# Optimization experiments

Measured on AMD Instinct MI355X. Metric: run time of the kernel, lower is better.

The kernel has to match this reference:

```python
import jax, jax.numpy as jnp
import numpy as np

B, T = 32, 48
INPUT_DIM = 40000
TRAJ = 10
H = 256
OUT = 40000
TD = 48
L = 2
E = 128
DIN = E + TD  # 176


def setup_inputs() -> dict:
    key = jax.random.key(0)
    ks = jax.random.split(key, 16)
    s = 0.05
    inp = {
        "locations": jax.random.randint(ks[0], (B, T), 0, INPUT_DIM),
        "times": jax.random.randint(ks[1], (B, T), 0, TD),
        "labels": jax.random.randint(ks[2], (B,), 0, TRAJ),
        "embed_table": jax.random.normal(ks[3], (INPUT_DIM, E), dtype=jnp.float32) * s,
        "traj_table": jax.random.normal(ks[4], (TRAJ, H * L), dtype=jnp.float32) * s,
        "fc_w": jax.random.normal(ks[5], (OUT + TD, H), dtype=jnp.float32) * s,
        "fc_b": jnp.zeros((OUT + TD,), dtype=jnp.float32),
        "w_ih0": jax.random.normal(ks[6], (3 * H, DIN), dtype=jnp.float32) * s,
        "w_hh0": jax.random.normal(ks[7], (3 * H, H), dtype=jnp.float32) * s,
        "b_ih0": jnp.zeros((3 * H,), dtype=jnp.float32),
        "b_hh0": jnp.zeros((3 * H,), dtype=jnp.float32),
        "w_ih1": jax.random.normal(ks[8], (3 * H, H), dtype=jnp.float32) * s,
        "w_hh1": jax.random.normal(ks[9], (3 * H, H), dtype=jnp.float32) * s,
        "b_ih1": jnp.zeros((3 * H,), dtype=jnp.float32),
        "b_hh1": jnp.zeros((3 * H,), dtype=jnp.float32),
    }
    return inp


def gru_layer(x, h0, w_ih, w_hh, b_ih, b_hh):
    """PyTorch-semantics GRU layer. x: [T,B,din], h0: [B,H] -> [T,B,H]."""
    # precompute input projections for all timesteps (gates ordered r,z,n)
    xp = jnp.einsum('tbd,gd->tbg', x, w_ih) + b_ih  # [T,B,3H]

    def step(h, xp_t):
        hp = h @ w_hh.T + b_hh                      # [B,3H]
        xr, xz, xn = jnp.split(xp_t, 3, axis=-1)
        hr, hz, hn = jnp.split(hp, 3, axis=-1)
        r = jax.nn.sigmoid(xr + hr)
        z = jax.nn.sigmoid(xz + hz)
        n = jnp.tanh(xn + r * hn)
        h_new = (1.0 - z) * n + z * h
        return h_new, h_new

    _, ys = jax.lax.scan(step, h0, xp)
    return ys


def reference(locations, times, labels, embed_table, traj_table, fc_w, fc_b,
              w_ih0, w_hh0, b_ih0, b_hh0, w_ih1, w_hh1, b_ih1, b_hh1):
    x = embed_table[locations]                                  # [B,T,E]
    th = jax.nn.one_hot(times, TD, dtype=x.dtype)               # [B,T,TD]
    x = jnp.concatenate([x, th], axis=-1).transpose(1, 0, 2)    # [T,B,E+TD]
    # init_hidden: view (B, L*H) -> (L, -1, H), a raw reshape as in torch
    h0 = traj_table[labels].reshape(L, -1, H)                   # [L,B,H]
    y = gru_layer(x, h0[0], w_ih0, w_hh0, b_ih0, b_hh0)
    y = gru_layer(y, h0[1], w_ih1, w_hh1, b_ih1, b_hh1)         # [T,B,H]
    out = jax.nn.relu(y).transpose(1, 0, 2) @ fc_w.T + fc_b     # [B,T,OUT+TD]
    loc = jax.nn.log_softmax(out[..., :OUT], axis=-1)
    tm = jax.nn.log_softmax(out[..., OUT:], axis=-1)
    return loc, tm
```

## Files before the change

### kernel.cpp

```cpp
#include <hip/hip_runtime.h>
#include <math.h>

typedef __attribute__((ext_vector_type(4))) float f32x4;
typedef __attribute__((ext_vector_type(8))) short s16x8;

constexpr int B = 32, T = 48, H = 256, E = 128, TD = 48;
constexpr int OUT = 40000, NOUTC = 40048, NPADC = 40064;
constexpr int G3 = 768, DIN = 176;

__device__ __forceinline__ float sigmoidf_(float x){ return 1.f/(1.f+__expf(-x)); }
__device__ __forceinline__ float tanhf_(float x){
  float e = __expf(2.f*x);
  return 1.f - 2.f/(e + 1.f);
}
__device__ __forceinline__ unsigned short f2bf(float f){
  unsigned int u = __float_as_uint(f);
  u += 0x7fffu + ((u>>16)&1u);
  return (unsigned short)(u>>16);
}
__device__ __forceinline__ s16x8 pack8(float4 u, float4 v){
  s16x8 r;
  r[0]=(short)f2bf(u.x); r[1]=(short)f2bf(u.y); r[2]=(short)f2bf(u.z); r[3]=(short)f2bf(u.w);
  r[4]=(short)f2bf(v.x); r[5]=(short)f2bf(v.y); r[6]=(short)f2bf(v.z); r[7]=(short)f2bf(v.w);
  return r;
}
__device__ __forceinline__ void gl_lds16(const unsigned short* g, unsigned short* l){
  __builtin_amdgcn_global_load_lds((const __attribute__((address_space(1))) void*)g,
                                   (__attribute__((address_space(3))) void*)l, 16, 0, 0);
}
__device__ __forceinline__ void st_sc(unsigned* p, unsigned v){
  __hip_atomic_store(p, v, __ATOMIC_RELAXED, __HIP_MEMORY_SCOPE_SYSTEM);
}
__device__ __forceinline__ unsigned long long ld_sc64(const unsigned long long* p){
  return __hip_atomic_load(p, __ATOMIC_RELAXED, __HIP_MEMORY_SCOPE_SYSTEM);
}

__global__ void wt_kernel(const float* __restrict__ w_ih0, float* __restrict__ wT,
                          unsigned* __restrict__ bar){
  int i = blockIdx.x*256 + threadIdx.x;
  if (blockIdx.x == 0 && threadIdx.x == 0)
    __hip_atomic_store(bar, 0u, __ATOMIC_RELAXED, __HIP_MEMORY_SCOPE_SYSTEM);
  if (i >= E*G3) return;
  int e = i / G3, g = i % G3;
  wT[i] = w_ih0[g*DIN + e];
}

__global__ void xp0_kernel(const int* __restrict__ locations, const int* __restrict__ times,
                           const float* __restrict__ embed, const float* __restrict__ wT,
                           const float* __restrict__ w_ih0, const float* __restrict__ b_ih0,
                           float* __restrict__ xp0)
{
  __shared__ float emb_s[16][E];
  __shared__ int tm_s[16];
  const int r0 = blockIdx.x * 16;
  const int tid = threadIdx.x;
  for (int i = tid; i < 16*E; i += 256) {
    int p = i >> 7, e = i & 127;
    int r = r0 + p; int t = r >> 5, b = r & 31;
    emb_s[p][e] = embed[(size_t)locations[b*T + t]*E + e];
  }
  if (tid < 16) {
    int r = r0 + tid; int t = r >> 5, b = r & 31;
    tm_s[tid] = times[b*T + t];
  }
  __syncthreads();
  const int g = tid;
  float acc[16][3];
  #pragma unroll
  for (int p=0;p<16;p++){acc[p][0]=0.f;acc[p][1]=0.f;acc[p][2]=0.f;}
  for (int e = 0; e < E; e += 4) {
    float w0_[4], w1_[4], w2_[4];
    #pragma unroll
    for (int i=0;i<4;i++){
      w0_[i]=wT[(e+i)*G3 + g];
      w1_[i]=wT[(e+i)*G3 + 256 + g];
      w2_[i]=wT[(e+i)*G3 + 512 + g];
    }
    #pragma unroll
    for (int p=0;p<16;p++){
      float4 ev = *(const float4*)&emb_s[p][e];
      acc[p][0] += ev.x*w0_[0]+ev.y*w0_[1]+ev.z*w0_[2]+ev.w*w0_[3];
      acc[p][1] += ev.x*w1_[0]+ev.y*w1_[1]+ev.z*w1_[2]+ev.w*w1_[3];
      acc[p][2] += ev.x*w2_[0]+ev.y*w2_[1]+ev.z*w2_[2]+ev.w*w2_[3];
    }
  }
  #pragma unroll
  for (int p=0;p<16;p++){
    int r = r0+p; int tt = tm_s[p];
    xp0[(size_t)r*G3 + g]       = acc[p][0] + b_ih0[g]     + w_ih0[g*DIN       + E + tt];
    xp0[(size_t)r*G3 + 256 + g] = acc[p][1] + b_ih0[g+256] + w_ih0[(g+256)*DIN + E + tt];
    xp0[(size_t)r*G3 + 512 + g] = acc[p][2] + b_ih0[g+512] + w_ih0[(g+512)*DIN + E + tt];
  }
}

struct GruArgs {
  const float* xp0; const float* traj; const int* labels;
  const float* w_hh0; const float* b_hh0;
  const float* w_ih1; const float* w_hh1; const float* b_ih1; const float* b_hh1;
  unsigned short* exch;
  unsigned* bar;
  unsigned short* abf;
};

__global__ void __launch_bounds__(384, 2) gru_kernel(GruArgs a)
{
  __shared__ unsigned short Ash[2][32*264];
  __shared__ float gl0[3*32*17];
  __shared__ float gl1[4*32*17];
  __shared__ float hF0[512];
  __shared__ float hF1[512];
  const int tid  = threadIdx.x;
  const int jt   = blockIdx.x;
  const int wv   = tid >> 6;
  const int lane = tid & 63;
  const int g    = wv % 3, mt = wv / 3;
  const int fn   = lane & 15;
  const int fq   = lane >> 4;
  unsigned* exch32 = (unsigned*)a.exch;

  const int row = g*256 + jt*16 + fn;
  s16x8 b0[8], b1[16];
  #pragma unroll
  for (int kk = 0; kk < 8; ++kk) {
    const float* p0 = a.w_hh0 + (size_t)row*H + kk*32 + fq*8;
    const float* p1 = a.w_ih1 + (size_t)row*H + kk*32 + fq*8;
    const float* p2 = a.w_hh1 + (size_t)row*H + kk*32 + fq*8;
    b0[kk]    = pack8(*(const float4*)p0, *(const float4*)(p0+4));
    b1[kk]    = pack8(*(const float4*)p1, *(const float4*)(p1+4));
    b1[kk+8]  = pack8(*(const float4*)p2, *(const float4*)(p2+4));
  }

  for (int i = tid; i < 2*B*H; i += 384) {
    int l = i >> 13, bb = (i >> 8) & 31, h = i & 255;
    float v = a.traj[(size_t)a.labels[l*16 + (bb>>1)]*512 + (bb&1)*256 + h];
    Ash[l][bb*264 + h] = f2bf(v);
  }
  if (tid < 256) {
    int b = tid >> 3, jp = tid & 7, j0 = jp*2, gj = jt*16 + j0;
    float v00 = a.traj[(size_t)a.labels[(b>>1)]*512      + (b&1)*256 + gj];
    float v01 = a.traj[(size_t)a.labels[(b>>1)]*512      + (b&1)*256 + gj+1];
    float v10 = a.traj[(size_t)a.labels[16 + (b>>1)]*512 + (b&1)*256 + gj];
    float v11 = a.traj[(size_t)a.labels[16 + (b>>1)]*512 + (b&1)*256 + gj+1];
    hF0[b*16+j0] = v00; hF0[b*16+j0+1] = v01;
    hF1[b*16+j0] = v10; hF1[b*16+j0+1] = v11;
    st_sc(&exch32[(1*2+1)*4096 + b*128 + jt*8 + jp],
          (unsigned)f2bf(v10) | ((unsigned)f2bf(v11) << 16));
  }

  for (int p = 0; p <= T; ++p) {
    const int cur = p & 1, nxt = cur ^ 1;
    if (p) {
      const unsigned long long* src = (const unsigned long long*)a.exch + (size_t)cur*4096;
      unsigned long long v[11];
      #pragma unroll
      for (int k = 0; k < 11; ++k) {
        int i = tid + k*384;
        if (i < 4096) v[k] = ld_sc64(&src[i]);
      }
      #pragma unroll
      for (int k = 0; k < 11; ++k) {
        int i = tid + k*384;
        if (i < 4096) {
          int st = i >> 11, bb = (i >> 6) & 31, k4 = (i & 63) << 2;
          *(unsigned long long*)&Ash[st][bb*264 + k4] = v[k];
        }
      }
    }
    __syncthreads();

    if (p < T) {
      f32x4 acc = (f32x4){0.f,0.f,0.f,0.f};
      #pragma unroll
      for (int kk = 0; kk < 8; ++kk) {
        s16x8 af = *(const s16x8*)&Ash[0][(mt*16 + fn)*264 + kk*32 + fq*8];
        acc = __builtin_amdgcn_mfma_f32_16x16x32_bf16(af, b0[kk], acc, 0, 0, 0);
      }
      #pragma unroll
      for (int i = 0; i < 4; ++i)
        gl0[(g*32 + mt*16 + fq*4 + i)*17 + fn] = acc[i];
    }
    if (p >= 1) {
      if (g < 2) {
        f32x4 acc = (f32x4){0.f,0.f,0.f,0.f};
        #pragma unroll
        for (int kk = 0; kk < 8; ++kk) {
          s16x8 af = *(const s16x8*)&Ash[0][(mt*16 + fn)*264 + kk*32 + fq*8];
          acc = __builtin_amdgcn_mfma_f32_16x16x32_bf16(af, b1[kk], acc, 0, 0, 0);
        }
        #pragma unroll
        for (int kk = 0; kk < 8; ++kk) {
          s16x8 af = *(const s16x8*)&Ash[1][(mt*16 + fn)*264 + kk*32 + fq*8];
          acc = __builtin_amdgcn_mfma_f32_16x16x32_bf16(af, b1[8+kk], acc, 0, 0, 0);
        }
        #pragma unroll
        for (int i = 0; i < 4; ++i)
          gl1[(g*32 + mt*16 + fq*4 + i)*17 + fn] = acc[i];
      } else {
        f32x4 ax = (f32x4){0.f,0.f,0.f,0.f}, ah = (f32x4){0.f,0.f,0.f,0.f};
        #pragma unroll
        for (int kk = 0; kk < 8; ++kk) {
          s16x8 afx = *(const s16x8*)&Ash[0][(mt*16 + fn)*264 + kk*32 + fq*8];
          s16x8 afh = *(const s16x8*)&Ash[1][(mt*16 + fn)*264 + kk*32 + fq*8];
          ax = __builtin_amdgcn_mfma_f32_16x16x32_bf16(afx, b1[kk],   ax, 0, 0, 0);
          ah = __builtin_amdgcn_mfma_f32_16x16x32_bf16(afh, b1[8+kk], ah, 0, 0, 0);
        }
        #pragma unroll
        for (int i = 0; i < 4; ++i) {
          gl1[(2*32 + mt*16 + fq*4 + i)*17 + fn] = ax[i];
          gl1[(3*32 + mt*16 + fq*4 + i)*17 + fn] = ah[i];
        }
      }
    }
    __syncthreads();

    if (tid < 256) {
      const int b = tid >> 3, jp = tid & 7, j0 = jp*2, gj = jt*16 + j0;
      if (p < T) {
        const float* xp = a.xp0 + (size_t)(p*B + b)*G3 + gj;
        float r0 = sigmoidf_(xp[0]   + gl0[(b)*17+j0]      + a.b_hh0[gj]);
        float r1 = sigmoidf_(xp[1]   + gl0[(b)*17+j0+1]    + a.b_hh0[gj+1]);
        float z0 = sigmoidf_(xp[256] + gl0[(32+b)*17+j0]   + a.b_hh0[256+gj]);
        float z1 = sigmoidf_(xp[257] + gl0[(32+b)*17+j0+1] + a.b_hh0[256+gj+1]);
        float n0 = tanhf_(xp[512] + r0*(gl0[(64+b)*17+j0]   + a.b_hh0[512+gj]));
        float n1 = tanhf_(xp[513] + r1*(gl0[(64+b)*17+j0+1] + a.b_hh0[512+gj+1]));
        float h0n = (1.f - z0)*n0 + z0*hF0[b*16+j0];
        float h1n = (1.f - z1)*n1 + z1*hF0[b*16+j0+1];
        hF0[b*16+j0] = h0n; hF0[b*16+j0+1] = h1n;
        st_sc(&exch32[(nxt*2 + 0)*4096 + b*128 + jt*8 + jp],
              (unsigned)f2bf(h0n) | ((unsigned)f2bf(h1n) << 16));
      }
      if (p >= 1) {
        const int t1 = p - 1;
        float r0 = sigmoidf_(gl1[(b)*17+j0]      + a.b_ih1[gj]     + a.b_hh1[gj]);
        float r1 = sigmoidf_(gl1[(b)*17+j0+1]    + a.b_ih1[gj+1]   + a.b_hh1[gj+1]);
        float z0 = sigmoidf_(gl1[(32+b)*17+j0]   + a.b_ih1[256+gj]   + a.b_hh1[256+gj]);
        float z1 = sigmoidf_(gl1[(32+b)*17+j0+1] + a.b_ih1[256+gj+1] + a.b_hh1[256+gj+1]);
        float n0 = tanhf_(gl1[(64+b)*17+j0]   + a.b_ih1[512+gj]
                          + r0*(gl1[(96+b)*17+j0]   + a.b_hh1[512+gj]));
        float n1 = tanhf_(gl1[(64+b)*17+j0+1] + a.b_ih1[512+gj+1]
                          + r1*(gl1[(96+b)*17+j0+1] + a.b_hh1[512+gj+1]));
        float h0n = (1.f - z0)*n0 + z0*hF1[b*16+j0];
        float h1n = (1.f - z1)*n1 + z1*hF1[b*16+j0+1];
        hF1[b*16+j0] = h0n; hF1[b*16+j0+1] = h1n;
        st_sc(&exch32[(nxt*2 + 1)*4096 + b*128 + jt*8 + jp],
              (unsigned)f2bf(h0n) | ((unsigned)f2bf(h1n) << 16));
        ((unsigned*)a.abf)[((size_t)(b*T + t1)*H + gj) >> 1] =
              (unsigned)f2bf(fmaxf(h0n,0.f)) | ((unsigned)f2bf(fmaxf(h1n,0.f)) << 16);
      }
    }
    if (p == T) break;

    asm volatile("s_waitcnt vmcnt(0)" ::: "memory");
    __syncthreads();
    if (tid == 0) {
      __hip_atomic_fetch_add(a.bar, 1u, __ATOMIC_RELAXED, __HIP_MEMORY_SCOPE_SYSTEM);
      const unsigned tgt = 16u*(unsigned)(p + 1);
      unsigned it = 0;
      while (__hip_atomic_load(a.bar, __ATOMIC_RELAXED, __HIP_MEMORY_SCOPE_SYSTEM) < tgt) {
        if (++it > (1u<<21)) break;
      }
    }
    __syncthreads();
  }
}

__global__ void castw_kernel(const float* __restrict__ fcw, unsigned short* __restrict__ wbf){
  int g = blockIdx.x*256 + threadIdx.x;
  if (g >= NPADC*64) return;
  int row = g >> 6;
  ushort4 o;
  if (row < NOUTC) {
    float4 v = ((const float4*)fcw)[g];
    o.x=f2bf(v.x); o.y=f2bf(v.y); o.z=f2bf(v.z); o.w=f2bf(v.w);
  } else { o.x=0; o.y=0; o.z=0; o.w=0; }
  ((ushort4*)wbf)[g] = o;
}

__global__ void __launch_bounds__(256) gemm_kernel(const unsigned short* __restrict__ Abf,
                                                   const unsigned short* __restrict__ Wbf,
                                                   const float* __restrict__ fc_b,
                                                   float* __restrict__ dout)
{
  __shared__ unsigned short As[128*32];
  __shared__ unsigned short Ws[128*32];
  const int m0 = blockIdx.x * 128;
  const int n0 = blockIdx.y * 128;
  const int tid = threadIdx.x;
  const int lane = tid & 63;
  const int wv = tid >> 6;
  f32x4 acc[2][8];
  #pragma unroll
  for (int i=0;i<2;i++)
    #pragma unroll
    for(int jx=0;jx<8;jx++) acc[i][jx] = (f32x4){0.f,0.f,0.f,0.f};

  const int srow = tid >> 2;
  const int skoff = (tid & 3) * 8;
  const unsigned short* aptr = Abf + (size_t)(m0 + srow)*256 + skoff;
  const unsigned short* wptr = Wbf + (size_t)(n0 + srow)*256 + skoff;
  unsigned short* asd = &As[tid*8];
  unsigned short* wsd = &Ws[tid*8];

  const int fr = lane & 15;
  const int fk = (lane >> 4) * 8;

  for (int kk = 0; kk < 256; kk += 32) {
    gl_lds16(aptr + kk,            asd);
    gl_lds16(aptr + 64*256 + kk,   asd + 64*32);
    gl_lds16(wptr + kk,            wsd);
    gl_lds16(wptr + 64*256 + kk,   wsd + 64*32);
    __syncthreads();
    s16x8 a0 = *(const s16x8*)&As[(wv*32 + fr)*32 + fk];
    s16x8 a1 = *(const s16x8*)&As[(wv*32 + 16 + fr)*32 + fk];
    #pragma unroll
    for (int ct = 0; ct < 8; ++ct) {
      s16x8 bfr = *(const s16x8*)&Ws[(ct*16 + fr)*32 + fk];
      acc[0][ct] = __builtin_amdgcn_mfma_f32_16x16x32_bf16(a0, bfr, acc[0][ct], 0, 0, 0);
      acc[1][ct] = __builtin_amdgcn_mfma_f32_16x16x32_bf16(a1, bfr, acc[1][ct], 0, 0, 0);
    }
    __syncthreads();
  }

  const int quad = lane >> 4;
  #pragma unroll
  for (int rt = 0; rt < 2; ++rt) {
    #pragma unroll
    for (int ct = 0; ct < 8; ++ct) {
      int col = n0 + ct*16 + fr;
      if (col < NOUTC) {
        float bias = fc_b[col];
        #pragma unroll
        for (int i = 0; i < 4; ++i) {
          int row = m0 + wv*32 + rt*16 + quad*4 + i;
          float v = acc[rt][ct][i] + bias;
          if (col < OUT) dout[(size_t)row*OUT + col] = v;
          else dout[(size_t)OUT*B*T + (size_t)row*TD + (col - OUT)] = v;
        }
      }
    }
  }
}

__global__ void stats_kernel(const float* __restrict__ dout, float* __restrict__ logz){
  const int r = blockIdx.x;
  const float4* row = (const float4*)(dout + (size_t)r*OUT);
  float m = -INFINITY, s = 0.f;
  for (int i = threadIdx.x; i < OUT/4; i += 256) {
    float4 v = row[i];
    float mx = fmaxf(fmaxf(v.x,v.y), fmaxf(v.z,v.w));
    if (mx > m) { s *= __expf(m - mx); m = mx; }
    s += __expf(v.x-m)+__expf(v.y-m)+__expf(v.z-m)+__expf(v.w-m);
  }
  #pragma unroll
  for (int off = 1; off < 64; off <<= 1) {
    float m2 = __shfl_xor(m, off);
    float s2 = __shfl_xor(s, off);
    float nm = fmaxf(m, m2);
    s = s*__expf(m-nm) + s2*__expf(m2-nm);
    m = nm;
  }
  __shared__ float sm[4], ss[4];
  if ((threadIdx.x & 63) == 0){ sm[threadIdx.x>>6]=m; ss[threadIdx.x>>6]=s; }
  __syncthreads();
  if (threadIdx.x == 0){
    float M=sm[0], S=ss[0];
    #pragma unroll
    for (int w=1;w<4;w++){
      float nm=fmaxf(M,sm[w]); S = S*__expf(M-nm)+ss[w]*__expf(sm[w]-nm); M=nm;
    }
    logz[r] = M + logf(S);
  }
}

__global__ void norm_kernel(float* __restrict__ dout, const float* __restrict__ logz){
  size_t i = (size_t)blockIdx.x*256 + threadIdx.x;
  if (i >= (size_t)B*T*OUT/4) return;
  int r = (int)(i / (OUT/4));
  float lz = logz[r];
  float4* p = (float4*)dout + i;
  float4 v = *p;
  v.x -= lz; v.y -= lz; v.z -= lz; v.w -= lz;
  *p = v;
}

__global__ void tm_kernel(float* __restrict__ dout){
  const int r = blockIdx.x;
  const int lane = threadIdx.x;
  float* base = dout + (size_t)OUT*B*T + (size_t)r*TD;
  float v = (lane < TD) ? base[lane] : -INFINITY;
  float m = v;
  #pragma unroll
  for (int off=32; off; off>>=1) m = fmaxf(m, __shfl_xor(m, off));
  float e = (lane < TD) ? __expf(v - m) : 0.f;
  float s = e;
  #pragma unroll
  for (int off=32; off; off>>=1) s += __shfl_xor(s, off);
  float lz = m + logf(s);
  if (lane < TD) base[lane] = v - lz;
}

extern "C" void kernel_launch(void* const* d_in, const int* in_sizes, int n_in,
                              void* d_out, int out_size, void* d_ws, size_t ws_size,
                              hipStream_t stream)
{
  const int*   locations = (const int*)d_in[0];
  const int*   times     = (const int*)d_in[1];
  const int*   labels    = (const int*)d_in[2];
  const float* embed     = (const float*)d_in[3];
  const float* traj      = (const float*)d_in[4];
  const float* fc_w      = (const float*)d_in[5];
  const float* fc_b      = (const float*)d_in[6];
  const float* w_ih0     = (const float*)d_in[7];
  const float* w_hh0     = (const float*)d_in[8];
  const float* b_ih0     = (const float*)d_in[9];
  const float* b_hh0     = (const float*)d_in[10];
  const float* w_ih1     = (const float*)d_in[11];
  const float* w_hh1     = (const float*)d_in[12];
  const float* b_ih1     = (const float*)d_in[13];
  const float* b_hh1     = (const float*)d_in[14];
  float* out = (float*)d_out;
  char* ws = (char*)d_ws;

  float* xp0            = (float*)(ws);
  unsigned short* exch  = (unsigned short*)(ws + 4718592);
  unsigned* bar         = (unsigned*)(ws + 4784128);
  float* logz           = (float*)(ws + 4784384);
  unsigned short* abf   = (unsigned short*)(ws + 4790528);
  unsigned short* wbf   = (unsigned short*)(ws + 5576960);
  float* wT             = (float*)(ws + 26089728);

  castw_kernel<<<dim3((NPADC*64 + 255)/256), dim3(256), 0, stream>>>(fc_w, wbf);
  wt_kernel<<<dim3((E*G3 + 255)/256), dim3(256), 0, stream>>>(w_ih0, wT, bar);
  xp0_kernel<<<dim3(96), dim3(256), 0, stream>>>(locations, times, embed, wT, w_ih0, b_ih0, xp0);

  GruArgs ga{xp0, traj, labels, w_hh0, b_hh0, w_ih1, w_hh1, b_ih1, b_hh1,
             exch, bar, abf};
  void* kargs[] = { &ga };
  hipLaunchCooperativeKernel((void*)gru_kernel, dim3(16), dim3(384), kargs, 0, stream);

  gemm_kernel<<<dim3(12, 313), dim3(256), 0, stream>>>(abf, wbf, fc_b, out);
  stats_kernel<<<dim3(B*T), dim3(256), 0, stream>>>(out, logz);
  norm_kernel<<<dim3((B*T*OUT/4 + 255)/256), dim3(256), 0, stream>>>(out, logz);
  tm_kernel<<<dim3(B*T), dim3(64), 0, stream>>>(out);
}
```

Before: 772.0 us.

## Replace GRU grid barrier with per-block flags and fuse softmax partials into GEMM

```diff
diff --git a/kernel.cpp b/kernel.cpp
--- a/kernel.cpp
+++ b/kernel.cpp
@@ -7,6 +7,7 @@
 constexpr int B = 32, T = 48, H = 256, E = 128, TD = 48;
 constexpr int OUT = 40000, NOUTC = 40048, NPADC = 40064;
 constexpr int G3 = 768, DIN = 176;
+constexpr int NT = 313, NTP = 320;
 
 __device__ __forceinline__ float sigmoidf_(float x){ return 1.f/(1.f+__expf(-x)); }
 __device__ __forceinline__ float tanhf_(float x){
@@ -31,15 +32,18 @@
 __device__ __forceinline__ void st_sc(unsigned* p, unsigned v){
   __hip_atomic_store(p, v, __ATOMIC_RELAXED, __HIP_MEMORY_SCOPE_SYSTEM);
 }
+__device__ __forceinline__ unsigned ld_sc32(const unsigned* p){
+  return __hip_atomic_load((unsigned*)p, __ATOMIC_RELAXED, __HIP_MEMORY_SCOPE_SYSTEM);
+}
 __device__ __forceinline__ unsigned long long ld_sc64(const unsigned long long* p){
-  return __hip_atomic_load(p, __ATOMIC_RELAXED, __HIP_MEMORY_SCOPE_SYSTEM);
+  return __hip_atomic_load((unsigned long long*)p, __ATOMIC_RELAXED, __HIP_MEMORY_SCOPE_SYSTEM);
 }
 
 __global__ void wt_kernel(const float* __restrict__ w_ih0, float* __restrict__ wT,
-                          unsigned* __restrict__ bar){
+                          unsigned* __restrict__ flags){
   int i = blockIdx.x*256 + threadIdx.x;
-  if (blockIdx.x == 0 && threadIdx.x == 0)
-    __hip_atomic_store(bar, 0u, __ATOMIC_RELAXED, __HIP_MEMORY_SCOPE_SYSTEM);
+  if (blockIdx.x == 0 && threadIdx.x < 32)
+    __hip_atomic_store(&flags[threadIdx.x], 0u, __ATOMIC_RELAXED, __HIP_MEMORY_SCOPE_SYSTEM);
   if (i >= E*G3) return;
   int e = i / G3, g = i % G3;
   wT[i] = w_ih0[g*DIN + e];
@@ -97,8 +101,8 @@
   const float* xp0; const float* traj; const int* labels;
   const float* w_hh0; const float* b_hh0;
   const float* w_ih1; const float* w_hh1; const float* b_ih1; const float* b_hh1;
-  unsigned short* exch;
-  unsigned* bar;
+  unsigned* exch;
+  unsigned* flags;
   unsigned short* abf;
 };
 
@@ -107,8 +111,6 @@
   __shared__ unsigned short Ash[2][32*264];
   __shared__ float gl0[3*32*17];
   __shared__ float gl1[4*32*17];
-  __shared__ float hF0[512];
-  __shared__ float hF1[512];
   const int tid  = threadIdx.x;
   const int jt   = blockIdx.x;
   const int wv   = tid >> 6;
@@ -116,7 +118,6 @@
   const int g    = wv % 3, mt = wv / 3;
   const int fn   = lane & 15;
   const int fq   = lane >> 4;
-  unsigned* exch32 = (unsigned*)a.exch;
 
   const int row = g*256 + jt*16 + fn;
   s16x8 b0[8], b1[16];
@@ -130,27 +131,56 @@
     b1[kk+8]  = pack8(*(const float4*)p2, *(const float4*)(p2+4));
   }
 
+  const int pb = tid >> 3, pjp = tid & 7, pj0 = pjp*2, pgj = jt*16 + pj0;
+  float2 bh0r, bh0z, bh0n, bi1r, bi1z, bi1n, bh1r, bh1z, bh1n;
+  float hc00 = 0.f, hc01 = 0.f, hc10 = 0.f, hc11 = 0.f;
+  if (tid < 256) {
+    bh0r = *(const float2*)&a.b_hh0[pgj];
+    bh0z = *(const float2*)&a.b_hh0[256+pgj];
+    bh0n = *(const float2*)&a.b_hh0[512+pgj];
+    bi1r = *(const float2*)&a.b_ih1[pgj];
+    bi1z = *(const float2*)&a.b_ih1[256+pgj];
+    bi1n = *(const float2*)&a.b_ih1[512+pgj];
+    bh1r = *(const float2*)&a.b_hh1[pgj];
+    bh1z = *(const float2*)&a.b_hh1[256+pgj];
+    bh1n = *(const float2*)&a.b_hh1[512+pgj];
+  }
+
   for (int i = tid; i < 2*B*H; i += 384) {
     int l = i >> 13, bb = (i >> 8) & 31, h = i & 255;
     float v = a.traj[(size_t)a.labels[l*16 + (bb>>1)]*512 + (bb&1)*256 + h];
     Ash[l][bb*264 + h] = f2bf(v);
   }
   if (tid < 256) {
-    int b = tid >> 3, jp = tid & 7, j0 = jp*2, gj = jt*16 + j0;
-    float v00 = a.traj[(size_t)a.labels[(b>>1)]*512      + (b&1)*256 + gj];
-    float v01 = a.traj[(size_t)a.labels[(b>>1)]*512      + (b&1)*256 + gj+1];
-    float v10 = a.traj[(size_t)a.labels[16 + (b>>1)]*512 + (b&1)*256 + gj];
-    float v11 = a.traj[(size_t)a.labels[16 + (b>>1)]*512 + (b&1)*256 + gj+1];
-    hF0[b*16+j0] = v00; hF0[b*16+j0+1] = v01;
-    hF1[b*16+j0] = v10; hF1[b*16+j0+1] = v11;
-    st_sc(&exch32[(1*2+1)*4096 + b*128 + jt*8 + jp],
+    float v00 = a.traj[(size_t)a.labels[(pb>>1)]*512      + (pb&1)*256 + pgj];
+    float v01 = a.traj[(size_t)a.labels[(pb>>1)]*512      + (pb&1)*256 + pgj+1];
+    float v10 = a.traj[(size_t)a.labels[16 + (pb>>1)]*512 + (pb&1)*256 + pgj];
+    float v11 = a.traj[(size_t)a.labels[16 + (pb>>1)]*512 + (pb&1)*256 + pgj+1];
+    hc00 = v00; hc01 = v01; hc10 = v10; hc11 = v11;
+    st_sc(&a.exch[1*8192 + ((jt*2 + 1)*32 + pb)*8 + pjp],
           (unsigned)f2bf(v10) | ((unsigned)f2bf(v11) << 16));
   }
 
   for (int p = 0; p <= T; ++p) {
-    const int cur = p & 1, nxt = cur ^ 1;
+    float2 xr, xz, xn;
+    if (p < T && tid < 256) {
+      const float* xp = a.xp0 + (size_t)(p*B + pb)*G3 + pgj;
+      xr = *(const float2*)(xp);
+      xz = *(const float2*)(xp + 256);
+      xn = *(const float2*)(xp + 512);
+    }
     if (p) {
-      const unsigned long long* src = (const unsigned long long*)a.exch + (size_t)cur*4096;
+      const unsigned want = (unsigned)p;
+      {
+        unsigned it = 0;
+        for (;;) {
+          unsigned f = want;
+          if (lane < 16) f = ld_sc32(&a.flags[(p & 1)*16 + lane]);
+          if (__all((int)(f >= want))) break;
+          if (++it > (1u << 22)) break;
+        }
+      }
+      const unsigned long long* src = (const unsigned long long*)a.exch + (size_t)(p & 1)*4096;
       unsigned long long v[11];
       #pragma unroll
       for (int k = 0; k < 11; ++k) {
@@ -161,8 +191,8 @@
       for (int k = 0; k < 11; ++k) {
         int i = tid + k*384;
         if (i < 4096) {
-          int st = i >> 11, bb = (i >> 6) & 31, k4 = (i & 63) << 2;
-          *(unsigned long long*)&Ash[st][bb*264 + k4] = v[k];
+          int pp = i & 3, bb = (i >> 2) & 31, st = (i >> 7) & 1, jtp = (i >> 8) & 15;
+          *(unsigned long long*)&Ash[st][bb*264 + jtp*16 + pp*4] = v[k];
         }
       }
     }
@@ -214,53 +244,44 @@
     __syncthreads();
 
     if (tid < 256) {
-      const int b = tid >> 3, jp = tid & 7, j0 = jp*2, gj = jt*16 + j0;
+      const int slot = (p + 1) & 1;
       if (p < T) {
-        const float* xp = a.xp0 + (size_t)(p*B + b)*G3 + gj;
-        float r0 = sigmoidf_(xp[0]   + gl0[(b)*17+j0]      + a.b_hh0[gj]);
-        float r1 = sigmoidf_(xp[1]   + gl0[(b)*17+j0+1]    + a.b_hh0[gj+1]);
-        float z0 = sigmoidf_(xp[256] + gl0[(32+b)*17+j0]   + a.b_hh0[256+gj]);
-        float z1 = sigmoidf_(xp[257] + gl0[(32+b)*17+j0+1] + a.b_hh0[256+gj+1]);
-        float n0 = tanhf_(xp[512] + r0*(gl0[(64+b)*17+j0]   + a.b_hh0[512+gj]));
-        float n1 = tanhf_(xp[513] + r1*(gl0[(64+b)*17+j0+1] + a.b_hh0[512+gj+1]));
-        float h0n = (1.f - z0)*n0 + z0*hF0[b*16+j0];
-        float h1n = (1.f - z1)*n1 + z1*hF0[b*16+j0+1];
-        hF0[b*16+j0] = h0n; hF0[b*16+j0+1] = h1n;
-        st_sc(&exch32[(nxt*2 + 0)*4096 + b*128 + jt*8 + jp],
+        float r0 = sigmoidf_(xr.x + gl0[pb*17+pj0]        + bh0r.x);
+        float r1 = sigmoidf_(xr.y + gl0[pb*17+pj0+1]      + bh0r.y);
+        float z0 = sigmoidf_(xz.x + gl0[(32+pb)*17+pj0]   + bh0z.x);
+        float z1 = sigmoidf_(xz.y + gl0[(32+pb)*17+pj0+1] + bh0z.y);
+        float n0 = tanhf_(xn.x + r0*(gl0[(64+pb)*17+pj0]   + bh0n.x));
+        float n1 = tanhf_(xn.y + r1*(gl0[(64+pb)*17+pj0+1] + bh0n.y));
+        float h0n = (1.f - z0)*n0 + z0*hc00;
+        float h1n = (1.f - z1)*n1 + z1*hc01;
+        hc00 = h0n; hc01 = h1n;
+        st_sc(&a.exch[(size_t)slot*8192 + ((jt*2 + 0)*32 + pb)*8 + pjp],
               (unsigned)f2bf(h0n) | ((unsigned)f2bf(h1n) << 16));
       }
       if (p >= 1) {
         const int t1 = p - 1;
-        float r0 = sigmoidf_(gl1[(b)*17+j0]      + a.b_ih1[gj]     + a.b_hh1[gj]);
-        float r1 = sigmoidf_(gl1[(b)*17+j0+1]    + a.b_ih1[gj+1]   + a.b_hh1[gj+1]);
-        float z0 = sigmoidf_(gl1[(32+b)*17+j0]   + a.b_ih1[256+gj]   + a.b_hh1[256+gj]);
-        float z1 = sigmoidf_(gl1[(32+b)*17+j0+1] + a.b_ih1[256+gj+1] + a.b_hh1[256+gj+1]);
-        float n0 = tanhf_(gl1[(64+b)*17+j0]   + a.b_ih1[512+gj]
-                          + r0*(gl1[(96+b)*17+j0]   + a.b_hh1[512+gj]));
-        float n1 = tanhf_(gl1[(64+b)*17+j0+1] + a.b_ih1[512+gj+1]
-                          + r1*(gl1[(96+b)*17+j0+1] + a.b_hh1[512+gj+1]));
-        float h0n = (1.f - z0)*n0 + z0*hF1[b*16+j0];
-        float h1n = (1.f - z1)*n1 + z1*hF1[b*16+j0+1];
-        hF1[b*16+j0] = h0n; hF1[b*16+j0+1] = h1n;
-        st_sc(&exch32[(nxt*2 + 1)*4096 + b*128 + jt*8 + jp],
-              (unsigned)f2bf(h0n) | ((unsigned)f2bf(h1n) << 16));
-        ((unsigned*)a.abf)[((size_t)(b*T + t1)*H + gj) >> 1] =
+        float r0 = sigmoidf_(gl1[pb*17+pj0]        + bi1r.x + bh1r.x);
+        float r1 = sigmoidf_(gl1[pb*17+pj0+1]      + bi1r.y + bh1r.y);
+        float z0 = sigmoidf_(gl1[(32+pb)*17+pj0]   + bi1z.x + bh1z.x);
+        float z1 = sigmoidf_(gl1[(32+pb)*17+pj0+1] + bi1z.y + bh1z.y);
+        float n0 = tanhf_(gl1[(64+pb)*17+pj0]   + bi1n.x + r0*(gl1[(96+pb)*17+pj0]   + bh1n.x));
+        float n1 = tanhf_(gl1[(64+pb)*17+pj0+1] + bi1n.y + r1*(gl1[(96+pb)*17+pj0+1] + bh1n.y));
+        float h0n = (1.f - z0)*n0 + z0*hc10;
+        float h1n = (1.f - z1)*n1 + z1*hc11;
+        hc10 = h0n; hc11 = h1n;
+        if (p < T)
+          st_sc(&a.exch[(size_t)slot*8192 + ((jt*2 + 1)*32 + pb)*8 + pjp],
+                (unsigned)f2bf(h0n) | ((unsigned)f2bf(h1n) << 16));
+        ((unsigned*)a.abf)[((size_t)(pb*T + t1)*H + pgj) >> 1] =
               (unsigned)f2bf(fmaxf(h0n,0.f)) | ((unsigned)f2bf(fmaxf(h1n,0.f)) << 16);
       }
     }
-    if (p == T) break;
-
-    asm volatile("s_waitcnt vmcnt(0)" ::: "memory");
-    __syncthreads();
-    if (tid == 0) {
-      __hip_atomic_fetch_add(a.bar, 1u, __ATOMIC_RELAXED, __HIP_MEMORY_SCOPE_SYSTEM);
-      const unsigned tgt = 16u*(unsigned)(p + 1);
-      unsigned it = 0;
-      while (__hip_atomic_load(a.bar, __ATOMIC_RELAXED, __HIP_MEMORY_SCOPE_SYSTEM) < tgt) {
-        if (++it > (1u<<21)) break;
-      }
-    }
-    __syncthreads();
+    if (p < T) {
+      asm volatile("s_waitcnt vmcnt(0)" ::: "memory");
+      __syncthreads();
+      if (tid == 0)
+        st_sc(&a.flags[((p + 1) & 1)*16 + jt], (unsigned)(p + 1));
+    }
   }
 }
 
@@ -279,7 +300,8 @@
 __global__ void __launch_bounds__(256) gemm_kernel(const unsigned short* __restrict__ Abf,
                                                    const unsigned short* __restrict__ Wbf,
                                                    const float* __restrict__ fc_b,
-                                                   float* __restrict__ dout)
+                                                   float* __restrict__ dout,
+                                                   float2* __restrict__ part)
 {
   __shared__ unsigned short As[128*32];
   __shared__ unsigned short Ws[128*32];
@@ -327,49 +349,63 @@
     #pragma unroll
     for (int ct = 0; ct < 8; ++ct) {
       int col = n0 + ct*16 + fr;
+      float bias = (col < NOUTC) ? fc_b[col] : 0.f;
+      #pragma unroll
+      for (int i = 0; i < 4; ++i) acc[rt][ct][i] += bias;
       if (col < NOUTC) {
-        float bias = fc_b[col];
         #pragma unroll
         for (int i = 0; i < 4; ++i) {
-          int row = m0 + wv*32 + rt*16 + quad*4 + i;
-          float v = acc[rt][ct][i] + bias;
-          if (col < OUT) dout[(size_t)row*OUT + col] = v;
-          else dout[(size_t)OUT*B*T + (size_t)row*TD + (col - OUT)] = v;
-        }
-      }
-    }
-  }
-}
-
-__global__ void stats_kernel(const float* __restrict__ dout, float* __restrict__ logz){
+          int row2 = m0 + wv*32 + rt*16 + quad*4 + i;
+          float v = acc[rt][ct][i];
+          if (col < OUT) dout[(size_t)row2*OUT + col] = v;
+          else dout[(size_t)OUT*B*T + (size_t)row2*TD + (col - OUT)] = v;
+        }
+      }
+    }
+  }
+  #pragma unroll
+  for (int rt = 0; rt < 2; ++rt) {
+    #pragma unroll
+    for (int i = 0; i < 4; ++i) {
+      float mx = -INFINITY;
+      #pragma unroll
+      for (int ct = 0; ct < 8; ++ct)
+        if (n0 + ct*16 + fr < OUT) mx = fmaxf(mx, acc[rt][ct][i]);
+      #pragma unroll
+      for (int off = 1; off < 16; off <<= 1) mx = fmaxf(mx, __shfl_xor(mx, off));
+      float sx = 0.f;
+      #pragma unroll
+      for (int ct = 0; ct < 8; ++ct)
+        if (n0 + ct*16 + fr < OUT) sx += __expf(acc[rt][ct][i] - mx);
+      #pragma unroll
+      for (int off = 1; off < 16; off <<= 1) sx += __shfl_xor(sx, off);
+      if (fr == 0) {
+        int row2 = m0 + wv*32 + rt*16 + quad*4 + i;
+        part[(size_t)row2*NTP + (n0 >> 7)] = make_float2(mx, sx);
+      }
+    }
+  }
+}
+
+__global__ void stats_kernel(const float2* __restrict__ part, float* __restrict__ logz){
   const int r = blockIdx.x;
-  const float4* row = (const float4*)(dout + (size_t)r*OUT);
+  const int lane = threadIdx.x;
   float m = -INFINITY, s = 0.f;
-  for (int i = threadIdx.x; i < OUT/4; i += 256) {
-    float4 v = row[i];
-    float mx = fmaxf(fmaxf(v.x,v.y), fmaxf(v.z,v.w));
-    if (mx > m) { s *= __expf(m - mx); m = mx; }
-    s += __expf(v.x-m)+__expf(v.y-m)+__expf(v.z-m)+__expf(v.w-m);
+  for (int i = lane; i < NT; i += 64) {
+    float2 pp = part[(size_t)r*NTP + i];
+    float nm = fmaxf(m, pp.x);
+    s = s*__expf(m - nm) + pp.y*__expf(pp.x - nm);
+    m = nm;
   }
   #pragma unroll
   for (int off = 1; off < 64; off <<= 1) {
     float m2 = __shfl_xor(m, off);
     float s2 = __shfl_xor(s, off);
     float nm = fmaxf(m, m2);
-    s = s*__expf(m-nm) + s2*__expf(m2-nm);
+    s = s*__expf(m - nm) + s2*__expf(m2 - nm);
     m = nm;
   }
-  __shared__ float sm[4], ss[4];
-  if ((threadIdx.x & 63) == 0){ sm[threadIdx.x>>6]=m; ss[threadIdx.x>>6]=s; }
-  __syncthreads();
-  if (threadIdx.x == 0){
-    float M=sm[0], S=ss[0];
-    #pragma unroll
-    for (int w=1;w<4;w++){
-      float nm=fmaxf(M,sm[w]); S = S*__expf(M-nm)+ss[w]*__expf(sm[w]-nm); M=nm;
-    }
-    logz[r] = M + logf(S);
-  }
+  if (lane == 0) logz[r] = m + logf(s);
 }
 
 __global__ void norm_kernel(float* __restrict__ dout, const float* __restrict__ logz){
@@ -422,24 +458,25 @@
   char* ws = (char*)d_ws;
 
   float* xp0            = (float*)(ws);
-  unsigned short* exch  = (unsigned short*)(ws + 4718592);
-  unsigned* bar         = (unsigned*)(ws + 4784128);
+  float2* part          = (float2*)(ws);
+  unsigned* exch        = (unsigned*)(ws + 4718592);
+  unsigned* flags       = (unsigned*)(ws + 4784128);
   float* logz           = (float*)(ws + 4784384);
   unsigned short* abf   = (unsigned short*)(ws + 4790528);
   unsigned short* wbf   = (unsigned short*)(ws + 5576960);
   float* wT             = (float*)(ws + 26089728);
 
   castw_kernel<<<dim3((NPADC*64 + 255)/256), dim3(256), 0, stream>>>(fc_w, wbf);
-  wt_kernel<<<dim3((E*G3 + 255)/256), dim3(256), 0, stream>>>(w_ih0, wT, bar);
+  wt_kernel<<<dim3((E*G3 + 255)/256), dim3(256), 0, stream>>>(w_ih0, wT, flags);
   xp0_kernel<<<dim3(96), dim3(256), 0, stream>>>(locations, times, embed, wT, w_ih0, b_ih0, xp0);
 
   GruArgs ga{xp0, traj, labels, w_hh0, b_hh0, w_ih1, w_hh1, b_ih1, b_hh1,
-             exch, bar, abf};
+             exch, flags, abf};
   void* kargs[] = { &ga };
   hipLaunchCooperativeKernel((void*)gru_kernel, dim3(16), dim3(384), kargs, 0, stream);
 
-  gemm_kernel<<<dim3(12, 313), dim3(256), 0, stream>>>(abf, wbf, fc_b, out);
-  stats_kernel<<<dim3(B*T), dim3(256), 0, stream>>>(out, logz);
+  gemm_kernel<<<dim3(12, 313), dim3(256), 0, stream>>>(abf, wbf, fc_b, out, part);
+  stats_kernel<<<dim3(B*T), dim3(64), 0, stream>>>(part, logz);
   norm_kernel<<<dim3((B*T*OUT/4 + 255)/256), dim3(256), 0, stream>>>(out, logz);
   tm_kernel<<<dim3(B*T), dim3(64), 0, stream>>>(out);
 }
```

Result: faster. 720.2 us (-6.7%).
